# Kernel optimization log

Measured on AMD Instinct MI355X. Metric: run time of the kernel, lower is better.

Reference implementation:

```python
import jax, jax.numpy as jnp
import numpy as np

NUM_HEADS = 8
NUM_GROUPS = 32
EPS = 1e-5


def group_norm(x, gamma, beta):
    b, c, h, w = x.shape
    xg = x.reshape(b, NUM_GROUPS, c // NUM_GROUPS, h, w)
    mean = jnp.mean(xg, axis=(2, 3, 4), keepdims=True)
    var = jnp.var(xg, axis=(2, 3, 4), keepdims=True)
    xn = ((xg - mean) * jax.lax.rsqrt(var + EPS)).reshape(b, c, h, w)
    return xn * gamma[None, :, None, None] + beta[None, :, None, None]


def setup_inputs() -> dict:
    key = jax.random.key(0)
    ks = jax.random.split(key, 4)
    b, c, h, w = 16, 512, 32, 32
    x = jax.random.normal(ks[0], (b, c, h, w), dtype=jnp.float32)
    gn_gamma = jnp.ones((c,), dtype=jnp.float32)
    gn_beta = jnp.zeros((c,), dtype=jnp.float32)
    qkv_w = jax.random.normal(ks[1], (3 * c, c), dtype=jnp.float32) * (1.0 / np.sqrt(c))
    qkv_b = jnp.zeros((3 * c,), dtype=jnp.float32)
    proj_w = jax.random.normal(ks[2], (c, c), dtype=jnp.float32) * (1.0 / np.sqrt(c))
    proj_b = jnp.zeros((c,), dtype=jnp.float32)
    return {"x": x, "gn_gamma": gn_gamma, "gn_beta": gn_beta,
            "qkv_w": qkv_w, "qkv_b": qkv_b, "proj_w": proj_w, "proj_b": proj_b}


def reference(x, gn_gamma, gn_beta, qkv_w, qkv_b, proj_w, proj_b):
    b, c, h, w = x.shape
    hd = c // NUM_HEADS
    hw = h * w

    xn = group_norm(x, gn_gamma, gn_beta)
    # 1x1 conv == channel matmul
    qkv = jnp.einsum('oc,bchw->bohw', qkv_w, xn) + qkv_b[None, :, None, None]
    q, k, v = jnp.split(qkv, 3, axis=1)
    q = q.reshape(b, NUM_HEADS, hd, hw)
    k = k.reshape(b, NUM_HEADS, hd, hw)
    v = v.reshape(b, NUM_HEADS, hd, hw)

    scale = 1.0 / np.sqrt(hd)
    attn = jnp.einsum('bhdt,bhds->bhts', q, k) * scale  # [b,H,hw,hw]
    attn = jax.nn.softmax(attn, axis=-1)
    h_attn = jnp.einsum('bhts,bhds->bhdt', attn, v).reshape(b, c, h, w)

    h_attn = jnp.einsum('oc,bchw->bohw', proj_w, h_attn) + proj_b[None, :, None, None]
    return x + h_attn
```

## Files before the change

kernel.cpp:

```cpp
#include <hip/hip_runtime.h>
#include <math.h>

#define NUM_HEADS 8
#define NUM_GROUPS 32
#define EPS 1e-5f

constexpr int B  = 16;
constexpr int C  = 512;
constexpr int HW = 1024;
constexpr int HD = 64;

typedef short bf16x8 __attribute__((ext_vector_type(8)));
typedef float f32x4  __attribute__((ext_vector_type(4)));

#define QSCALE 0.1803368801111f

__device__ inline unsigned short f2bf(float f) {
    union { float f; unsigned int u; } v; v.f = f;
    unsigned int r = (v.u + 0x7FFFu + ((v.u >> 16) & 1u)) >> 16;
    return (unsigned short)r;
}

__device__ __forceinline__ unsigned int pack_trunc(float lo, float hi) {
    return __builtin_amdgcn_perm(__float_as_uint(hi), __float_as_uint(lo), 0x07060302u);
}

__device__ __forceinline__ float exp2_raw(float x) {
#if __has_builtin(__builtin_amdgcn_exp2f)
    return __builtin_amdgcn_exp2f(x);
#else
    float r; asm("v_exp_f32 %0, %1" : "=v"(r) : "v"(x)); return r;
#endif
}

__device__ __forceinline__ void gld_lds16(void* lds, const void* g) {
    __builtin_amdgcn_global_load_lds(
        (const __attribute__((address_space(1))) void*)g,
        (__attribute__((address_space(3))) void*)lds, 16, 0, 0);
}

__device__ __forceinline__ void pl32_swap(unsigned int& a, unsigned int& b) {
#if __has_builtin(__builtin_amdgcn_permlane32_swap)
    auto r = __builtin_amdgcn_permlane32_swap(a, b, false, false);
    a = r[0]; b = r[1];
#else
    asm volatile("v_permlane32_swap_b32 %0, %1" : "+v"(a), "+v"(b));
#endif
}
__device__ __forceinline__ void pl16_swap(unsigned int& a, unsigned int& b) {
#if __has_builtin(__builtin_amdgcn_permlane16_swap)
    auto r = __builtin_amdgcn_permlane16_swap(a, b, false, false);
    a = r[0]; b = r[1];
#else
    asm volatile("v_permlane16_swap_b32 %0, %1" : "+v"(a), "+v"(b));
#endif
}

#define ABAR(VM) do {                                                   \
    asm volatile("s_waitcnt vmcnt(" VM ")\n\ts_barrier" ::: "memory");  \
    __builtin_amdgcn_sched_barrier(0);                                  \
} while (0)

__global__ __launch_bounds__(256)
void fused_pre_kernel(const float* __restrict__ x,
                      const float* __restrict__ gamma,
                      const float* __restrict__ beta,
                      unsigned short* __restrict__ xnT,
                      const float* __restrict__ qkv_w,
                      const float* __restrict__ proj_w,
                      unsigned short* __restrict__ wqb) {
    if (blockIdx.x >= 512) {
        const int i = (blockIdx.x - 512) * 256 + threadIdx.x;
        const int n1 = 786432 / 4;
        const int nt = 1048576 / 4;
        if (i >= nt) return;
        const float4 v = (i < n1) ? ((const float4*)qkv_w)[i]
                                  : ((const float4*)proj_w)[i - n1];
        ushort4 r;
        r.x = f2bf(v.x); r.y = f2bf(v.y); r.z = f2bf(v.z); r.w = f2bf(v.w);
        ((ushort4*)wqb)[i] = r;
        return;
    }
    const int bg = blockIdx.x;
    const int b = bg >> 5, g = bg & 31;
    const size_t base = ((size_t)b * C + (size_t)g * 16) * HW;
    const int hw0 = threadIdx.x * 4;

    float4 v4[16];
    float sum = 0.f, sumsq = 0.f;
    #pragma unroll
    for (int cl = 0; cl < 16; ++cl) {
        const float4 f = *(const float4*)(x + base + (size_t)cl * HW + hw0);
        v4[cl] = f;
        sum   += (f.x + f.y) + (f.z + f.w);
        sumsq += (f.x * f.x + f.y * f.y) + (f.z * f.z + f.w * f.w);
    }
    #pragma unroll
    for (int off = 32; off > 0; off >>= 1) {
        sum   += __shfl_down(sum, off, 64);
        sumsq += __shfl_down(sumsq, off, 64);
    }
    __shared__ float s_sum[4], s_sq[4];
    const int wid = threadIdx.x >> 6, lane = threadIdx.x & 63;
    if (lane == 0) { s_sum[wid] = sum; s_sq[wid] = sumsq; }
    __syncthreads();
    const float tsum = s_sum[0] + s_sum[1] + s_sum[2] + s_sum[3];
    const float tsq  = s_sq[0] + s_sq[1] + s_sq[2] + s_sq[3];
    const float mean = tsum * (1.0f / 16384.f);
    const float var  = tsq * (1.0f / 16384.f) - mean * mean;
    const float rstd = rsqrtf(var + EPS);

    float ga[16], be[16];
    #pragma unroll
    for (int cl = 0; cl < 16; ++cl) {
        ga[cl] = gamma[g * 16 + cl] * rstd;
        be[cl] = beta[g * 16 + cl] - mean * ga[cl];
    }

    #pragma unroll
    for (int j = 0; j < 4; ++j) {
        const int t = hw0 + j;
        unsigned short pk[16];
        #pragma unroll
        for (int cl = 0; cl < 16; ++cl) {
            const float f = (j == 0) ? v4[cl].x : (j == 1) ? v4[cl].y
                          : (j == 2) ? v4[cl].z : v4[cl].w;
            pk[cl] = f2bf(f * ga[cl] + be[cl]);
        }
        unsigned short* dst = xnT + ((size_t)(b * 1024 + t)) * 512 + g * 16;
        *(uint4*)dst = *(const uint4*)pk;
        *(uint4*)(dst + 8) = *(const uint4*)(pk + 8);
    }
}

__device__ __forceinline__ void gemm_stage(const char* __restrict__ Ab,
                                           const char* __restrict__ Bb,
                                           int step, unsigned short* As,
                                           unsigned short* Bs,
                                           int w, int lrow, int lkc) {
    #pragma unroll
    for (int i = 0; i < 2; ++i) {
        const int row = w * 32 + i * 16 + lrow;
        const int kc = lkc ^ ((row >> 1) & 3);
        const size_t goff = (size_t)row * 1024 + (size_t)step * 64 + kc * 16;
        gld_lds16((char*)As + w * 2048 + i * 1024, Ab + goff);
        gld_lds16((char*)Bs + w * 2048 + i * 1024, Bb + goff);
    }
}

__device__ __forceinline__ void gemm_step(const unsigned short* __restrict__ As,
                                          const unsigned short* __restrict__ Bs,
                                          f32x4 acc[4][4],
                                          int lo, int q4, int wm, int wn) {
    bf16x8 af[4], bfr[4];
    #pragma unroll
    for (int i = 0; i < 4; ++i) {
        const int ra = wm * 64 + i * 16 + lo;
        af[i]  = *(const bf16x8*)(As + ra * 32 + (q4 ^ ((ra >> 1) & 3)) * 8);
        const int rb = wn * 64 + i * 16 + lo;
        bfr[i] = *(const bf16x8*)(Bs + rb * 32 + (q4 ^ ((rb >> 1) & 3)) * 8);
    }
    __builtin_amdgcn_s_setprio(1);
    #pragma unroll
    for (int mi = 0; mi < 4; ++mi)
        #pragma unroll
        for (int ni = 0; ni < 4; ++ni)
            acc[mi][ni] = __builtin_amdgcn_mfma_f32_16x16x32_bf16(
                af[mi], bfr[ni], acc[mi][ni], 0, 0, 0);
    __builtin_amdgcn_s_setprio(0);
}

__device__ __forceinline__ void mfma_gemm_pipe(const char* __restrict__ Ab,
                                               const char* __restrict__ Bb,
                                               unsigned short* S,
                                               f32x4 acc[4][4]) {
    const int tid = threadIdx.x;
    const int w = tid >> 6, lane = tid & 63;
    const int lo = lane & 15, q4 = lane >> 4;
    const int wm = w >> 1, wn = w & 1;
    const int lrow = lane >> 2, lkc = lane & 3;

    unsigned short* A0 = S;             unsigned short* B0 = S + 4096;
    unsigned short* A1 = S + 8192;      unsigned short* B1 = S + 12288;
    unsigned short* A2 = S + 16384;     unsigned short* B2 = S + 20480;

    gemm_stage(Ab, Bb, 0, A0, B0, w, lrow, lkc);
    gemm_stage(Ab, Bb, 1, A1, B1, w, lrow, lkc);
    ABAR("4");
    gemm_stage(Ab, Bb, 2, A2, B2, w, lrow, lkc);
    gemm_step(A0, B0, acc, lo, q4, wm, wn);

    #pragma unroll 1
    for (int ii = 0; ii < 4; ++ii) {
        const int i = 3 * ii + 1;
        ABAR("4");
        gemm_stage(Ab, Bb, i + 2, A0, B0, w, lrow, lkc);
        gemm_step(A1, B1, acc, lo, q4, wm, wn);
        ABAR("4");
        gemm_stage(Ab, Bb, i + 3, A1, B1, w, lrow, lkc);
        gemm_step(A2, B2, acc, lo, q4, wm, wn);
        ABAR("4");
        gemm_stage(Ab, Bb, i + 4, A2, B2, w, lrow, lkc);
        gemm_step(A0, B0, acc, lo, q4, wm, wn);
    }

    ABAR("4");
    gemm_stage(Ab, Bb, 15, A0, B0, w, lrow, lkc);
    gemm_step(A1, B1, acc, lo, q4, wm, wn);
    ABAR("4");
    gemm_step(A2, B2, acc, lo, q4, wm, wn);
    ABAR("0");
    gemm_step(A0, B0, acc, lo, q4, wm, wn);
}

__global__ __launch_bounds__(256)
void qkv_mfma_kernel(const unsigned short* __restrict__ wqb,
                     const unsigned short* __restrict__ xnT,
                     const float* __restrict__ qkv_b,
                     unsigned short* __restrict__ Qt,
                     unsigned short* __restrict__ Kt,
                     unsigned short* __restrict__ Vb) {
    __shared__ __align__(16) unsigned short SMEM[3 * 8192];
    const int hw_id = blockIdx.x;
    const int wk = (hw_id % 192) * 8 + hw_id / 192;
    const int bx = wk & 7;
    const int by = (wk >> 3) % 12;
    const int batch = wk / 96;
    const int mBase = by * 128, nBase = bx * 128;

    f32x4 acc[4][4] = {};
    mfma_gemm_pipe((const char*)(wqb + (size_t)mBase * 512),
                   (const char*)(xnT + ((size_t)batch * 1024 + nBase) * 512),
                   SMEM, acc);

    const int tid = threadIdx.x;
    const int w = tid >> 6, lane = tid & 63;
    const int lo = lane & 15, q4 = lane >> 4;
    const int wm = w >> 1, wn = w & 1;
    const int mw = mBase + wm * 64;
    const int tb = nBase + wn * 64;

    __syncthreads();

    if (mw < 1024) {
        const bool isQ = mw < 512;
        const int head = (mw >> 6) & 7;
        unsigned short* dst = (isQ ? Qt : Kt) + (((size_t)batch * 8 + head) << 16);
        const float sc = isQ ? QSCALE : 1.0f;
        #pragma unroll
        for (int mi = 0; mi < 4; ++mi) {
            const float4 bq = *(const float4*)(qkv_b + mw + mi * 16 + q4 * 4);
            #pragma unroll
            for (int ni = 0; ni < 4; ++ni) {
                const int t = tb + ni * 16 + lo;
                ushort4 pk;
                pk.x = f2bf((acc[mi][ni][0] + bq.x) * sc);
                pk.y = f2bf((acc[mi][ni][1] + bq.y) * sc);
                pk.z = f2bf((acc[mi][ni][2] + bq.z) * sc);
                pk.w = f2bf((acc[mi][ni][3] + bq.w) * sc);
                *(ushort4*)(dst + (size_t)t * 64 + mi * 16 + q4 * 4) = pk;
            }
        }
    } else {
        unsigned short* T = SMEM + w * 2048;
        unsigned short* Vrow = Vb + (size_t)batch * 524288 + (size_t)(mw - 1024) * 1024 + tb;
        const int rl8 = lane >> 3, c8 = lane & 7;
        #pragma unroll
        for (int p = 0; p < 2; ++p) {
            #pragma unroll
            for (int mi2 = 0; mi2 < 2; ++mi2) {
                const int mi = 2 * p + mi2;
                const float4 bq = *(const float4*)(qkv_b + mw + mi * 16 + q4 * 4);
                const int dl = mi2 * 16 + q4 * 4;
                #pragma unroll
                for (int ni = 0; ni < 4; ++ni) {
                    const int tl = ni * 16 + lo;
                    T[(dl + 0) * 64 + tl] = f2bf(acc[mi][ni][0] + bq.x);
                    T[(dl + 1) * 64 + tl] = f2bf(acc[mi][ni][1] + bq.y);
                    T[(dl + 2) * 64 + tl] = f2bf(acc[mi][ni][2] + bq.z);
                    T[(dl + 3) * 64 + tl] = f2bf(acc[mi][ni][3] + bq.w);
                }
            }
            #pragma unroll
            for (int i = 0; i < 4; ++i) {
                const int dl = i * 8 + rl8;
                const uint4 val = *(const uint4*)&T[dl * 64 + c8 * 8];
                *(uint4*)(Vrow + (size_t)(p * 32 + dl) * 1024 + c8 * 8) = val;
            }
        }
    }
}

__device__ __forceinline__ void attn_stage(const unsigned short* __restrict__ Kp,
                                           const unsigned short* __restrict__ Vp,
                                           int s0, unsigned short* Kd,
                                           unsigned short* Vd,
                                           int w, int rl, int p8) {
    #pragma unroll
    for (int cc = 0; cc < 2; ++cc) {
        const int r = 16 * w + 8 * cc + rl;
        const int jj = p8 ^ (r & 7);
        gld_lds16(Kd + (16 * w + 8 * cc) * 64, Kp + (size_t)(s0 + r) * 64 + jj * 8);
        gld_lds16(Vd + (16 * w + 8 * cc) * 64, Vp + (size_t)r * 1024 + s0 + jj * 8);
    }
}

__device__ __forceinline__ void attn_chunk(const unsigned short* __restrict__ Kc,
                                           const unsigned short* __restrict__ Vc,
                                           const bf16x8 (&qf)[2][2],
                                           const bf16x8 ones,
                                           f32x4 (&oacc)[4][2], f32x4 (&lacc)[2],
                                           int lo, int q4, int xr) {
    f32x4 sacc[4][2] = {};
    __builtin_amdgcn_s_setprio(1);
    #pragma unroll
    for (int mt = 0; mt < 4; ++mt) {
        const unsigned short* kr = Kc + (16 * mt + lo) * 64;
        const bf16x8 a0 = *(const bf16x8*)(kr + ((q4    ) ^ xr) * 8);
        const bf16x8 a1 = *(const bf16x8*)(kr + ((q4 + 4) ^ xr) * 8);
        #pragma unroll
        for (int nt = 0; nt < 2; ++nt) {
            sacc[mt][nt] = __builtin_amdgcn_mfma_f32_16x16x32_bf16(a0, qf[nt][0], sacc[mt][nt], 0, 0, 0);
            sacc[mt][nt] = __builtin_amdgcn_mfma_f32_16x16x32_bf16(a1, qf[nt][1], sacc[mt][nt], 0, 0, 0);
        }
    }
    __builtin_amdgcn_s_setprio(0);

    bf16x8 bp[2][2];
    #pragma unroll
    for (int nt = 0; nt < 2; ++nt) {
        unsigned int X[4][2];
        #pragma unroll
        for (int mt = 0; mt < 4; ++mt) {
            const f32x4 s = sacc[mt][nt];
            const float p0 = exp2_raw(s[0]);
            const float p1 = exp2_raw(s[1]);
            const float p2 = exp2_raw(s[2]);
            const float p3 = exp2_raw(s[3]);
            X[mt][0] = pack_trunc(p0, p1);
            X[mt][1] = pack_trunc(p2, p3);
        }
        #pragma unroll
        for (int h2 = 0; h2 < 2; ++h2) {
            unsigned int Y0, Y1, Y2, Y3;
            {
                unsigned int a = X[2 * h2][0], bb = X[2 * h2 + 1][0];
                pl32_swap(a, bb);
                pl16_swap(a, bb);
                Y0 = a; Y2 = bb;
            }
            {
                unsigned int a = X[2 * h2][1], bb = X[2 * h2 + 1][1];
                pl32_swap(a, bb);
                pl16_swap(a, bb);
                Y1 = a; Y3 = bb;
            }
            union { unsigned int u[4]; bf16x8 v; } cv;
            cv.u[0] = Y0; cv.u[1] = Y1; cv.u[2] = Y2; cv.u[3] = Y3;
            bp[nt][h2] = cv.v;
        }
    }

    __builtin_amdgcn_s_setprio(1);
    #pragma unroll
    for (int nt = 0; nt < 2; ++nt) {
        lacc[nt] = __builtin_amdgcn_mfma_f32_16x16x32_bf16(ones, bp[nt][0], lacc[nt], 0, 0, 0);
        lacc[nt] = __builtin_amdgcn_mfma_f32_16x16x32_bf16(ones, bp[nt][1], lacc[nt], 0, 0, 0);
    }
    #pragma unroll
    for (int md = 0; md < 4; ++md) {
        const unsigned short* vr = Vc + (16 * md + lo) * 64;
        const bf16x8 v0 = *(const bf16x8*)(vr + ((q4    ) ^ xr) * 8);
        const bf16x8 v1 = *(const bf16x8*)(vr + ((q4 + 4) ^ xr) * 8);
        #pragma unroll
        for (int nt = 0; nt < 2; ++nt) {
            oacc[md][nt] = __builtin_amdgcn_mfma_f32_16x16x32_bf16(v0, bp[nt][0], oacc[md][nt], 0, 0, 0);
            oacc[md][nt] = __builtin_amdgcn_mfma_f32_16x16x32_bf16(v1, bp[nt][1], oacc[md][nt], 0, 0, 0);
        }
    }
    __builtin_amdgcn_s_setprio(0);
}

__global__ __launch_bounds__(256, 3)
void attn_mfma_kernel(const unsigned short* __restrict__ Qt,
                      const unsigned short* __restrict__ Kt,
                      const unsigned short* __restrict__ Vb,
                      unsigned short* __restrict__ attnT) {
    const int bh = blockIdx.x;
    const int b = bh >> 3, h = bh & 7;
    const int tBase = blockIdx.y * 128;
    const int tid = threadIdx.x;
    const int w = tid >> 6, lane = tid & 63;
    const int lo = lane & 15, q4 = lane >> 4;
    const int xr = lo & 7;

    __shared__ __align__(16) unsigned short Ks[3][64 * 64];
    __shared__ __align__(16) unsigned short Vs[3][64 * 64];

    const unsigned short* Kp = Kt + ((size_t)bh << 16);
    const unsigned short* Vp = Vb + ((size_t)b * 512 + h * 64) * 1024;

    bf16x8 qf[2][2];
    {
        const unsigned short* Qp = Qt + ((size_t)bh * 1024 + tBase + 32 * w) * 64;
        #pragma unroll
        for (int nt = 0; nt < 2; ++nt) {
            qf[nt][0] = *(const bf16x8*)(Qp + (size_t)(16 * nt + lo) * 64 + 8 * q4);
            qf[nt][1] = *(const bf16x8*)(Qp + (size_t)(16 * nt + lo) * 64 + 32 + 8 * q4);
        }
    }

    bf16x8 ones;
    #pragma unroll
    for (int i = 0; i < 8; ++i) ones[i] = (short)0x3F80;

    const int rl = lane >> 3, p8 = lane & 7;

    f32x4 oacc[4][2] = {};
    f32x4 lacc[2] = {};

    attn_stage(Kp, Vp, 0 * 64, Ks[0], Vs[0], w, rl, p8);
    attn_stage(Kp, Vp, 1 * 64, Ks[1], Vs[1], w, rl, p8);

    ABAR("4");
    attn_stage(Kp, Vp, 2 * 64, Ks[2], Vs[2], w, rl, p8);
    attn_chunk(Ks[0], Vs[0], qf, ones, oacc, lacc, lo, q4, xr);

    #pragma unroll 1
    for (int ii = 0; ii < 4; ++ii) {
        const int i = 3 * ii + 1;
        ABAR("4");
        attn_stage(Kp, Vp, (i + 2) * 64, Ks[0], Vs[0], w, rl, p8);
        attn_chunk(Ks[1], Vs[1], qf, ones, oacc, lacc, lo, q4, xr);
        ABAR("4");
        attn_stage(Kp, Vp, (i + 3) * 64, Ks[1], Vs[1], w, rl, p8);
        attn_chunk(Ks[2], Vs[2], qf, ones, oacc, lacc, lo, q4, xr);
        ABAR("4");
        attn_stage(Kp, Vp, (i + 4) * 64, Ks[2], Vs[2], w, rl, p8);
        attn_chunk(Ks[0], Vs[0], qf, ones, oacc, lacc, lo, q4, xr);
    }

    ABAR("4");
    attn_stage(Kp, Vp, 15 * 64, Ks[0], Vs[0], w, rl, p8);
    attn_chunk(Ks[1], Vs[1], qf, ones, oacc, lacc, lo, q4, xr);
    ABAR("4");
    attn_chunk(Ks[2], Vs[2], qf, ones, oacc, lacc, lo, q4, xr);
    ABAR("0");
    attn_chunk(Ks[0], Vs[0], qf, ones, oacc, lacc, lo, q4, xr);

    #pragma unroll
    for (int nt = 0; nt < 2; ++nt) {
        const float inv = 1.0f / lacc[nt][0];
        const int t = tBase + 32 * w + 16 * nt + lo;
        unsigned short* op = attnT + ((size_t)(b * 1024 + t)) * 512 + h * 64;
        #pragma unroll
        for (int md = 0; md < 4; ++md) {
            uint2 pk;
            pk.x = pack_trunc(oacc[md][nt][0] * inv, oacc[md][nt][1] * inv);
            pk.y = pack_trunc(oacc[md][nt][2] * inv, oacc[md][nt][3] * inv);
            *(uint2*)(op + 16 * md + 4 * q4) = pk;
        }
    }
}

__global__ __launch_bounds__(256)
void proj_mfma_kernel(const unsigned short* __restrict__ wpb,
                      const unsigned short* __restrict__ attnT,
                      const float* __restrict__ proj_b,
                      const float* __restrict__ x,
                      float* __restrict__ out) {
    __shared__ __align__(16) unsigned short SMEM[3 * 8192];
    const int hw_id = blockIdx.x;
    const int wk = (hw_id % 64) * 8 + hw_id / 64;
    const int bx = wk & 7;
    const int by = (wk >> 3) & 3;
    const int batch = wk >> 5;
    const int mBase = by * 128, nBase = bx * 128;

    f32x4 acc[4][4] = {};
    mfma_gemm_pipe((const char*)(wpb + (size_t)mBase * 512),
                   (const char*)(attnT + ((size_t)batch * 1024 + nBase) * 512),
                   SMEM, acc);

    const int tid = threadIdx.x;
    const int w = tid >> 6, lane = tid & 63;
    const int lo = lane & 15, q4 = lane >> 4;
    const int wm = w >> 1, wn = w & 1;
    const float* xb = x + (size_t)batch * 524288;
    float* ob = out + (size_t)batch * 524288;

    #pragma unroll
    for (int mi = 0; mi < 4; ++mi) {
        const int m0 = mBase + wm * 64 + mi * 16 + q4 * 4;
        const float4 bq = *(const float4*)(proj_b + m0);
        #pragma unroll
        for (int ni = 0; ni < 4; ++ni) {
            const int t = nBase + wn * 64 + ni * 16 + lo;
            const size_t o0 = (size_t)m0 * 1024 + t;
            ob[o0]          = acc[mi][ni][0] + bq.x + xb[o0];
            ob[o0 + 1024]   = acc[mi][ni][1] + bq.y + xb[o0 + 1024];
            ob[o0 + 2048]   = acc[mi][ni][2] + bq.z + xb[o0 + 2048];
            ob[o0 + 3072]   = acc[mi][ni][3] + bq.w + xb[o0 + 3072];
        }
    }
}

extern "C" void kernel_launch(void* const* d_in, const int* in_sizes, int n_in,
                              void* d_out, int out_size, void* d_ws, size_t ws_size,
                              hipStream_t stream) {
    const float* x        = (const float*)d_in[0];
    const float* gn_gamma = (const float*)d_in[1];
    const float* gn_beta  = (const float*)d_in[2];
    const float* qkv_w    = (const float*)d_in[3];
    const float* qkv_b    = (const float*)d_in[4];
    const float* proj_w   = (const float*)d_in[5];
    const float* proj_b   = (const float*)d_in[6];
    float* out = (float*)d_out;

    char* wsc = (char*)d_ws;
    unsigned short* xnT   = (unsigned short*)(wsc);
    unsigned short* Qt    = (unsigned short*)(wsc + 16777216);
    unsigned short* Kt    = (unsigned short*)(wsc + 33554432);
    unsigned short* Vb    = (unsigned short*)(wsc + 50331648);
    unsigned short* attnT = (unsigned short*)(wsc + 67108864);
    unsigned short* wqb   = (unsigned short*)(wsc + 83886080);
    unsigned short* wpb   = wqb + 786432;

    fused_pre_kernel<<<1536, 256, 0, stream>>>(x, gn_gamma, gn_beta, xnT,
                                               qkv_w, proj_w, wqb);

    qkv_mfma_kernel<<<1536, 256, 0, stream>>>(wqb, xnT, qkv_b, Qt, Kt, Vb);

    {
        dim3 grid(B * NUM_HEADS, HW / 128);
        attn_mfma_kernel<<<grid, 256, 0, stream>>>(Qt, Kt, Vb, attnT);
    }

    proj_mfma_kernel<<<512, 256, 0, stream>>>(wpb, attnT, proj_b, x, out);
}
```

Before: 200.8 us.

## Software-pipeline attention: overlap QK of next chunk with PV of previous

Splits the per-chunk attention step into QK, softmax-exp and PV phases and staggers them so each iteration computes QK for chunk i+1 while doing PV for chunk i. K and V staging are decoupled, with V loaded one chunk behind K to match the staggered use. This aims to hide exp/packing latency and MFMA dependency stalls behind independent matrix work. It costs extra live registers (sacc and bp carried across iterations) and a more intricate barrier and wait-count schedule, which raises occupancy and correctness risk.

Result: no change. 199.3 us (-0.7%).

```diff
diff --git a/kernel.cpp b/kernel.cpp
--- a/kernel.cpp
+++ b/kernel.cpp
@@ -291,27 +291,36 @@
     }
 }
 
-__device__ __forceinline__ void attn_stage(const unsigned short* __restrict__ Kp,
-                                           const unsigned short* __restrict__ Vp,
-                                           int s0, unsigned short* Kd,
-                                           unsigned short* Vd,
-                                           int w, int rl, int p8) {
+__device__ __forceinline__ void stage_K2(const unsigned short* __restrict__ Kp,
+                                         int s0, unsigned short* Kd,
+                                         int w, int rl, int p8) {
     #pragma unroll
     for (int cc = 0; cc < 2; ++cc) {
         const int r = 16 * w + 8 * cc + rl;
         const int jj = p8 ^ (r & 7);
         gld_lds16(Kd + (16 * w + 8 * cc) * 64, Kp + (size_t)(s0 + r) * 64 + jj * 8);
+    }
+}
+__device__ __forceinline__ void stage_V2(const unsigned short* __restrict__ Vp,
+                                         int s0, unsigned short* Vd,
+                                         int w, int rl, int p8) {
+    #pragma unroll
+    for (int cc = 0; cc < 2; ++cc) {
+        const int r = 16 * w + 8 * cc + rl;
+        const int jj = p8 ^ (r & 7);
         gld_lds16(Vd + (16 * w + 8 * cc) * 64, Vp + (size_t)r * 1024 + s0 + jj * 8);
     }
 }
 
-__device__ __forceinline__ void attn_chunk(const unsigned short* __restrict__ Kc,
-                                           const unsigned short* __restrict__ Vc,
-                                           const bf16x8 (&qf)[2][2],
-                                           const bf16x8 ones,
-                                           f32x4 (&oacc)[4][2], f32x4 (&lacc)[2],
-                                           int lo, int q4, int xr) {
-    f32x4 sacc[4][2] = {};
+__device__ __forceinline__ void attn_qk(const unsigned short* __restrict__ Kc,
+                                        const bf16x8 (&qf)[2][2],
+                                        f32x4 (&sacc)[4][2],
+                                        int lo, int q4, int xr) {
+    #pragma unroll
+    for (int mt = 0; mt < 4; ++mt)
+        #pragma unroll
+        for (int nt = 0; nt < 2; ++nt)
+            sacc[mt][nt] = f32x4{0.f, 0.f, 0.f, 0.f};
     __builtin_amdgcn_s_setprio(1);
     #pragma unroll
     for (int mt = 0; mt < 4; ++mt) {
@@ -325,8 +334,10 @@
         }
     }
     __builtin_amdgcn_s_setprio(0);
-
-    bf16x8 bp[2][2];
+}
+
+__device__ __forceinline__ void attn_sm(const f32x4 (&sacc)[4][2],
+                                        bf16x8 (&bp)[2][2]) {
     #pragma unroll
     for (int nt = 0; nt < 2; ++nt) {
         unsigned int X[4][2];
@@ -360,7 +371,13 @@
             bp[nt][h2] = cv.v;
         }
     }
-
+}
+
+__device__ __forceinline__ void attn_pv(const unsigned short* __restrict__ Vc,
+                                        const bf16x8 (&bp)[2][2],
+                                        const bf16x8 ones,
+                                        f32x4 (&oacc)[4][2], f32x4 (&lacc)[2],
+                                        int lo, int q4, int xr) {
     __builtin_amdgcn_s_setprio(1);
     #pragma unroll
     for (int nt = 0; nt < 2; ++nt) {
@@ -418,35 +435,59 @@
 
     f32x4 oacc[4][2] = {};
     f32x4 lacc[2] = {};
-
-    attn_stage(Kp, Vp, 0 * 64, Ks[0], Vs[0], w, rl, p8);
-    attn_stage(Kp, Vp, 1 * 64, Ks[1], Vs[1], w, rl, p8);
+    f32x4 sacc[4][2];
+    bf16x8 bp[2][2];
+
+    stage_K2(Kp, 0 * 64, Ks[0], w, rl, p8);
+    stage_K2(Kp, 1 * 64, Ks[1], w, rl, p8);
+    stage_V2(Vp, 0 * 64, Vs[0], w, rl, p8);
 
     ABAR("4");
-    attn_stage(Kp, Vp, 2 * 64, Ks[2], Vs[2], w, rl, p8);
-    attn_chunk(Ks[0], Vs[0], qf, ones, oacc, lacc, lo, q4, xr);
+    stage_K2(Kp, 2 * 64, Ks[2], w, rl, p8);
+    attn_qk(Ks[0], qf, sacc, lo, q4, xr);
+    stage_V2(Vp, 1 * 64, Vs[1], w, rl, p8);
+    attn_sm(sacc, bp);
 
     #pragma unroll 1
     for (int ii = 0; ii < 4; ++ii) {
         const int i = 3 * ii + 1;
         ABAR("4");
-        attn_stage(Kp, Vp, (i + 2) * 64, Ks[0], Vs[0], w, rl, p8);
-        attn_chunk(Ks[1], Vs[1], qf, ones, oacc, lacc, lo, q4, xr);
+        stage_K2(Kp, (i + 2) * 64, Ks[0], w, rl, p8);
+        attn_qk(Ks[1], qf, sacc, lo, q4, xr);
+        attn_pv(Vs[0], bp, ones, oacc, lacc, lo, q4, xr);
+        stage_V2(Vp, (i + 1) * 64, Vs[2], w, rl, p8);
+        attn_sm(sacc, bp);
         ABAR("4");
-        attn_stage(Kp, Vp, (i + 3) * 64, Ks[1], Vs[1], w, rl, p8);
-        attn_chunk(Ks[2], Vs[2], qf, ones, oacc, lacc, lo, q4, xr);
+        stage_K2(Kp, (i + 3) * 64, Ks[1], w, rl, p8);
+        attn_qk(Ks[2], qf, sacc, lo, q4, xr);
+        attn_pv(Vs[1], bp, ones, oacc, lacc, lo, q4, xr);
+        stage_V2(Vp, (i + 2) * 64, Vs[0], w, rl, p8);
+        attn_sm(sacc, bp);
         ABAR("4");
-        attn_stage(Kp, Vp, (i + 4) * 64, Ks[2], Vs[2], w, rl, p8);
-        attn_chunk(Ks[0], Vs[0], qf, ones, oacc, lacc, lo, q4, xr);
+        stage_K2(Kp, (i + 4) * 64, Ks[2], w, rl, p8);
+        attn_qk(Ks[0], qf, sacc, lo, q4, xr);
+        attn_pv(Vs[2], bp, ones, oacc, lacc, lo, q4, xr);
+        stage_V2(Vp, (i + 3) * 64, Vs[1], w, rl, p8);
+        attn_sm(sacc, bp);
     }
 
     ABAR("4");
-    attn_stage(Kp, Vp, 15 * 64, Ks[0], Vs[0], w, rl, p8);
-    attn_chunk(Ks[1], Vs[1], qf, ones, oacc, lacc, lo, q4, xr);
+    stage_K2(Kp, 15 * 64, Ks[0], w, rl, p8);
+    attn_qk(Ks[1], qf, sacc, lo, q4, xr);
+    attn_pv(Vs[0], bp, ones, oacc, lacc, lo, q4, xr);
+    stage_V2(Vp, 14 * 64, Vs[2], w, rl, p8);
+    attn_sm(sacc, bp);
     ABAR("4");
-    attn_chunk(Ks[2], Vs[2], qf, ones, oacc, lacc, lo, q4, xr);
+    attn_qk(Ks[2], qf, sacc, lo, q4, xr);
+    attn_pv(Vs[1], bp, ones, oacc, lacc, lo, q4, xr);
+    stage_V2(Vp, 15 * 64, Vs[0], w, rl, p8);
+    attn_sm(sacc, bp);
+    ABAR("2");
+    attn_qk(Ks[0], qf, sacc, lo, q4, xr);
+    attn_pv(Vs[2], bp, ones, oacc, lacc, lo, q4, xr);
+    attn_sm(sacc, bp);
     ABAR("0");
-    attn_chunk(Ks[0], Vs[0], qf, ones, oacc, lacc, lo, q4, xr);
+    attn_pv(Vs[0], bp, ones, oacc, lacc, lo, q4, xr);
 
     #pragma unroll
     for (int nt = 0; nt < 2; ++nt) {
```
